# Kernel optimization log

Hardware: AMD Instinct MI355X
Metric: run time of the kernel (lower is better)

## Reference

```python
import jax, jax.numpy as jnp
import numpy as np

NUM_BLOCKS = 4
SPARSITY = 0.01
SCALE = 0.02


def _softshrink(x, lambd):
    return jnp.where(x > lambd, x - lambd, jnp.where(x < -lambd, x + lambd, 0.0))


def setup_inputs() -> dict:
    key = jax.random.key(0)
    k = jax.random.split(key, 5)
    B, N, C = 8, 4096, 768
    bs = C // NUM_BLOCKS
    return {
        "x": jax.random.normal(k[0], (B, N, C), dtype=jnp.float32),
        "complex_weight_1": jax.random.normal(k[1], (2, NUM_BLOCKS, bs, bs), dtype=jnp.float32) * SCALE,
        "complex_bias_1": jax.random.normal(k[2], (2, NUM_BLOCKS, bs), dtype=jnp.float32) * SCALE,
        "complex_weight_2": jax.random.normal(k[3], (2, NUM_BLOCKS, bs, bs), dtype=jnp.float32) * SCALE,
        "complex_bias_2": jax.random.normal(k[4], (2, NUM_BLOCKS, bs), dtype=jnp.float32) * SCALE,
    }


def reference(x, complex_weight_1, complex_bias_1, complex_weight_2, complex_bias_2):
    B, N, C = x.shape
    bs = C // NUM_BLOCKS
    xb = x.reshape(B, N, NUM_BLOCKS, bs)
    # FFT over (seq, block) axes, ortho norm -> complex64
    xf = jnp.fft.fft2(xb, axes=(1, 2), norm="ortho")

    mul = lambda t, w: jnp.einsum("snbd,bdk->snbk", t, w)

    w1, b1 = complex_weight_1, complex_bias_1
    w2, b2 = complex_weight_2, complex_bias_2

    xr, xi = xf.real, xf.imag
    r1 = jax.nn.relu(mul(xr, w1[0]) - mul(xi, w1[1]) + b1[0])
    i1 = jax.nn.relu(mul(xr, w1[1]) + mul(xi, w1[0]) + b1[1])
    r2 = mul(r1, w2[0]) - mul(i1, w2[1]) + b2[0]
    i2 = mul(r1, w2[1]) + mul(i1, w2[0]) + b2[1]

    r2 = _softshrink(r2, SPARSITY)
    i2 = _softshrink(i2, SPARSITY)

    z = jax.lax.complex(r2, i2)
    out = jnp.fft.ifft2(z, axes=(1, 2), norm="ortho").real.astype(jnp.float32)
    return out.reshape(B, N, C)
```

## Files before the change

kernel.cpp:

```cpp
#include <hip/hip_runtime.h>
#include <math.h>

#define N_SEQ   4096
#define C_TOT   768
#define NBLK    4
#define BS      192
#define B_BATCH 8
#define LAMBDA  0.01f
#define KTOT    384
#define APITCH  392
#define SW(x)   ((x) ^ (((x) >> 5) & 31))

typedef short    bf16x8  __attribute__((ext_vector_type(8)));
typedef short    short4v __attribute__((ext_vector_type(4)));
typedef float    f32x4   __attribute__((ext_vector_type(4)));
typedef unsigned short ushort_t;

__device__ __forceinline__ unsigned short f2bf(float f) {
  unsigned int u = __float_as_uint(f);
  u = (u + 0x7FFFu + ((u >> 16) & 1u)) >> 16;
  return (unsigned short)u;
}
__device__ __forceinline__ float b2f(unsigned short h) {
  return __uint_as_float(((unsigned int)h) << 16);
}

__device__ __forceinline__ void stockham_soa4(float* Ar, float* Ai,
                                              float* Br, float* Bi,
                                              int t, float sign) {
  float *sr = Ar, *si = Ai, *dr = Br, *di = Bi;
  float inv_p = 1.0f;
  int p = 1;
#pragma unroll
  for (int s = 0; s < 6; s++) {
#pragma unroll
    for (int m = 0; m < 2; m++) {
      int i = t + m * 512;
      int k = i & (p - 1);
      float a0r = sr[SW(i)],        a0i = si[SW(i)];
      float a1r = sr[SW(i + 1024)], a1i = si[SW(i + 1024)];
      float a2r = sr[SW(i + 2048)], a2i = si[SW(i + 2048)];
      float a3r = sr[SW(i + 3072)], a3i = si[SW(i + 3072)];
      float ang = sign * 1.5707963268f * inv_p * (float)k;
      float s1, c1;
      __sincosf(ang, &s1, &c1);
      float c2 = c1 * c1 - s1 * s1, s2 = 2.0f * c1 * s1;
      float c3 = c1 * c2 - s1 * s2, s3 = c1 * s2 + s1 * c2;
      float b1r = c1 * a1r - s1 * a1i, b1i = c1 * a1i + s1 * a1r;
      float b2r = c2 * a2r - s2 * a2i, b2i = c2 * a2i + s2 * a2r;
      float b3r = c3 * a3r - s3 * a3i, b3i = c3 * a3i + s3 * a3r;
      float t0r = a0r + b2r, t0i = a0i + b2i;
      float t1r = a0r - b2r, t1i = a0i - b2i;
      float t2r = b1r + b3r, t2i = b1i + b3i;
      float t3r = b1r - b3r, t3i = b1i - b3i;
      int j = ((i - k) << 2) + k;
      dr[SW(j)]         = t0r + t2r;        di[SW(j)]         = t0i + t2i;
      dr[SW(j + p)]     = t1r - sign * t3i; di[SW(j + p)]     = t1i + sign * t3r;
      dr[SW(j + 2 * p)] = t0r - t2r;        di[SW(j + 2 * p)] = t0i - t2i;
      dr[SW(j + 3 * p)] = t1r + sign * t3i; di[SW(j + 3 * p)] = t1i - sign * t3r;
    }
    __syncthreads();
    float* tp;
    tp = sr; sr = dr; dr = tp;
    tp = si; si = di; di = tp;
    p <<= 2;
    inv_p *= 0.25f;
  }
}

__global__ __launch_bounds__(256) void transpose_kernel(
    const float* __restrict__ src, float* __restrict__ dst, int R, int C) {
  __shared__ float tile[64][65];
  const int c0 = blockIdx.x * 64, r0 = blockIdx.y * 64, b = blockIdx.z;
  const int tid = threadIdx.x;
#pragma unroll
  for (int it = 0; it < 4; it++) {
    int g = it * 256 + tid;
    int r = g >> 4, q = g & 15;
    float4 v = *(const float4*)(src + ((size_t)b * R + r0 + r) * C + c0 + q * 4);
    tile[q * 4 + 0][r] = v.x;
    tile[q * 4 + 1][r] = v.y;
    tile[q * 4 + 2][r] = v.z;
    tile[q * 4 + 3][r] = v.w;
  }
  __syncthreads();
#pragma unroll
  for (int it = 0; it < 4; it++) {
    int g = it * 256 + tid;
    int c = g >> 4, w = g & 15;
    float4 v = make_float4(tile[c][w * 4 + 0], tile[c][w * 4 + 1],
                           tile[c][w * 4 + 2], tile[c][w * 4 + 3]);
    *(float4*)(dst + ((size_t)b * C + c0 + c) * R + r0 + w * 4) = v;
  }
}

__global__ __launch_bounds__(256) void prep_kernel(
    const float* __restrict__ w1, const float* __restrict__ w2,
    ushort_t* __restrict__ Bc) {
  int idx = blockIdx.x * 256 + threadIdx.x;
  int layer = idx / 589824; int r = idx - layer * 589824;
  int kb = r / 147456;      int r2 = r - kb * 147456;
  int jc = r2 / 6144;       int r3 = r2 - jc * 6144;
  int kc = r3 / 512;        int r4 = r3 - kc * 512;
  int lane = r4 >> 3;       int e = r4 & 7;
  int j = jc * 16 + (lane & 15);
  int k = kc * 32 + (lane >> 4) * 8 + e;
  const float* w = layer ? w2 : w1;
  float v;
  if (k < 192) {
    v = (j < 192) ? w[(kb * 192 + k) * 192 + j]
                  : w[((4 + kb) * 192 + k) * 192 + (j - 192)];
  } else {
    int k2 = k - 192;
    v = (j < 192) ? -w[((4 + kb) * 192 + k2) * 192 + j]
                  :  w[(kb * 192 + k2) * 192 + (j - 192)];
  }
  Bc[idx] = f2bf(v);
}

__global__ __launch_bounds__(512) void fft_fwd_kernel(
    const float* __restrict__ xT, ushort_t* __restrict__ Fr,
    ushort_t* __restrict__ Fi) {
  __shared__ float Ar[N_SEQ], Ai[N_SEQ], Br[N_SEQ], Bi[N_SEQ];
  const int q = blockIdx.x, b = blockIdx.y;
  const int c1 = 2 * q;
  const int t = threadIdx.x;
  const float* p1 = xT + ((size_t)b * C_TOT + c1) * N_SEQ;
  const float* p2 = p1 + N_SEQ;
#pragma unroll
  for (int m = 0; m < 8; m++) {
    int i = t + m * 512;
    Ar[SW(i)] = p1[i];
    Ai[SW(i)] = p2[i];
  }
  __syncthreads();
  stockham_soa4(Ar, Ai, Br, Bi, t, -1.0f);
  ushort_t* fr1 = Fr + ((size_t)b * C_TOT + c1) * N_SEQ;
  ushort_t* fi1 = Fi + ((size_t)b * C_TOT + c1) * N_SEQ;
#pragma unroll
  for (int m = 0; m < 8; m++) {
    int k = t + m * 512;
    int km = (N_SEQ - k) & (N_SEQ - 1);
    float a = Ar[SW(k)], bb = Ai[SW(k)], c = Ar[SW(km)], d = Ai[SW(km)];
    fr1[k]         = f2bf(0.5f * (a + c));
    fi1[k]         = f2bf(0.5f * (bb - d));
    fr1[N_SEQ + k] = f2bf(0.5f * (bb + d));
    fi1[N_SEQ + k] = f2bf(0.5f * (c - a));
  }
}

__global__ __launch_bounds__(256, 3) void mlp_kernel(
    const ushort_t* __restrict__ Fr, const ushort_t* __restrict__ Fi,
    const ushort_t* __restrict__ Bc,
    const float* __restrict__ b1g, const float* __restrict__ b2g,
    ushort_t* __restrict__ Or, ushort_t* __restrict__ Oi) {
  __shared__ ushort_t Abuf[64 * APITCH];
  const int nt = blockIdx.x, kb = blockIdx.y, b = blockIdx.z;
  const int n0 = nt * 64;
  const int tid = threadIdx.x;
  const int lane = tid & 63, wave = tid >> 6;
  const int fr = lane & 15, fg = lane >> 4;
  const int col0 = wave * 96;

  {
    const size_t S = (size_t)BS * N_SEQ;
    const float s = 0.0078125f;
#pragma unroll
    for (int it = 0; it < 6; it++) {
      int g = it * 256 + tid;
      int d = g >> 3, n8 = g & 7;
      size_t bse = ((size_t)(b * C_TOT + d)) * N_SEQ + n0 + n8 * 8;
      bf16x8 y0r = *(const bf16x8*)(Fr + bse);
      bf16x8 y0i = *(const bf16x8*)(Fi + bse);
      bf16x8 y1r = *(const bf16x8*)(Fr + bse + S);
      bf16x8 y1i = *(const bf16x8*)(Fi + bse + S);
      bf16x8 y2r = *(const bf16x8*)(Fr + bse + 2 * S);
      bf16x8 y2i = *(const bf16x8*)(Fi + bse + 2 * S);
      bf16x8 y3r = *(const bf16x8*)(Fr + bse + 3 * S);
      bf16x8 y3i = *(const bf16x8*)(Fi + bse + 3 * S);
#pragma unroll
      for (int e = 0; e < 8; e++) {
        float a0r = b2f((unsigned short)y0r[e]), a0i = b2f((unsigned short)y0i[e]);
        float a1r = b2f((unsigned short)y1r[e]), a1i = b2f((unsigned short)y1i[e]);
        float a2r = b2f((unsigned short)y2r[e]), a2i = b2f((unsigned short)y2i[e]);
        float a3r = b2f((unsigned short)y3r[e]), a3i = b2f((unsigned short)y3i[e]);
        float zr, zi;
        if (kb == 0)      { zr = a0r + a1r + a2r + a3r; zi = a0i + a1i + a2i + a3i; }
        else if (kb == 1) { zr = a0r + a1i - a2r - a3i; zi = a0i - a1r - a2i + a3r; }
        else if (kb == 2) { zr = a0r - a1r + a2r - a3r; zi = a0i - a1i + a2i - a3i; }
        else              { zr = a0r - a1i - a2r + a3i; zi = a0i + a1r - a2i - a3r; }
        int n = n8 * 8 + e;
        Abuf[n * APITCH + d]       = f2bf(zr * s);
        Abuf[n * APITCH + 192 + d] = f2bf(zi * s);
      }
    }
  }
  __syncthreads();

  const ushort_t* B1 = Bc + (size_t)kb * 147456 + (size_t)wave * 36864 +
                       (size_t)lane * 8;
  const ushort_t* B2 = B1 + 589824;

  f32x4 acc[4][6];
  bf16x8 bf0[6], bf1[6], afr[4];

  auto loadB = [&](const ushort_t* Bb, int kc, bf16x8* dst) {
#pragma unroll
    for (int ct = 0; ct < 6; ct++)
      dst[ct] = *(const bf16x8*)(Bb + (size_t)kc * 512 + ct * 6144);
  };
  auto doK = [&](int kc, bf16x8* bw) {
#pragma unroll
    for (int rt = 0; rt < 4; rt++)
      afr[rt] = *(const bf16x8*)(&Abuf[(rt * 16 + fr) * APITCH + kc * 32 + fg * 8]);
#pragma unroll
    for (int rt = 0; rt < 4; rt++)
#pragma unroll
      for (int ct = 0; ct < 6; ct++)
        acc[rt][ct] = __builtin_amdgcn_mfma_f32_16x16x32_bf16(
            afr[rt], bw[ct], acc[rt][ct], 0, 0, 0);
  };

#pragma unroll
  for (int rt = 0; rt < 4; rt++)
#pragma unroll
    for (int ct = 0; ct < 6; ct++) acc[rt][ct] = 0.0f;
  loadB(B1, 0, bf0);
#pragma unroll
  for (int kc2 = 0; kc2 < 6; kc2++) {
    loadB(B1, 2 * kc2 + 1, bf1);
    doK(2 * kc2, bf0);
    if (kc2 < 5) loadB(B1, 2 * kc2 + 2, bf0);
    doK(2 * kc2 + 1, bf1);
  }

  __syncthreads();
#pragma unroll
  for (int ct = 0; ct < 6; ct++) {
    int j = col0 + ct * 16 + fr;
    float bias = (j < 192) ? b1g[kb * 192 + j] : b1g[768 + kb * 192 + (j - 192)];
#pragma unroll
    for (int rt = 0; rt < 4; rt++)
#pragma unroll
      for (int reg = 0; reg < 4; reg++) {
        float v = acc[rt][ct][reg] + bias;
        v = fmaxf(v, 0.0f);
        Abuf[(rt * 16 + fg * 4 + reg) * APITCH + j] = f2bf(v);
      }
  }
  __syncthreads();

#pragma unroll
  for (int rt = 0; rt < 4; rt++)
#pragma unroll
    for (int ct = 0; ct < 6; ct++) acc[rt][ct] = 0.0f;
  loadB(B2, 0, bf0);
#pragma unroll
  for (int kc2 = 0; kc2 < 6; kc2++) {
    loadB(B2, 2 * kc2 + 1, bf1);
    doK(2 * kc2, bf0);
    if (kc2 < 5) loadB(B2, 2 * kc2 + 2, bf0);
    doK(2 * kc2 + 1, bf1);
  }

#pragma unroll
  for (int ct = 0; ct < 6; ct++) {
    int j = col0 + ct * 16 + fr;
    float bias;
    ushort_t* plane;
    if (j < 192) {
      bias = b2g[kb * 192 + j];
      plane = Or + ((size_t)(b * C_TOT + kb * 192 + j)) * N_SEQ;
    } else {
      bias = b2g[768 + kb * 192 + (j - 192)];
      plane = Oi + ((size_t)(b * C_TOT + kb * 192 + (j - 192))) * N_SEQ;
    }
#pragma unroll
    for (int rt = 0; rt < 4; rt++) {
      short4v pk;
#pragma unroll
      for (int reg = 0; reg < 4; reg++) {
        float v = acc[rt][ct][reg] + bias;
        v = (v > LAMBDA) ? (v - LAMBDA) : ((v < -LAMBDA) ? (v + LAMBDA) : 0.0f);
        pk[reg] = (short)f2bf(v);
      }
      *(short4v*)(plane + n0 + rt * 16 + fg * 4) = pk;
    }
  }
}

__global__ __launch_bounds__(512) void fft_inv_kernel(
    const ushort_t* __restrict__ Or, const ushort_t* __restrict__ Oi,
    float* __restrict__ yT) {
  __shared__ float Ar[N_SEQ], Ai[N_SEQ], Br[N_SEQ], Bi[N_SEQ];
  const int q = blockIdx.x, b = blockIdx.y;
  const int c1 = 2 * q;
  const int jb = c1 / 192;
  const int d  = c1 - jb * 192;
  const int t = threadIdx.x;
  const size_t S = (size_t)BS * N_SEQ;
  const float s = 1.0f / 128.0f;
  const size_t base0 = ((size_t)b * C_TOT + d) * N_SEQ;
#pragma unroll
  for (int m = 0; m < 2; m++) {
    int i0 = m * 2048 + t * 4;
#pragma unroll
    for (int col = 0; col < 2; col++) {
      size_t bse = base0 + (size_t)col * N_SEQ + i0;
      short4v z0r = *(const short4v*)(Or + bse);
      short4v z0i = *(const short4v*)(Oi + bse);
      short4v z1r = *(const short4v*)(Or + bse + S);
      short4v z1i = *(const short4v*)(Oi + bse + S);
      short4v z2r = *(const short4v*)(Or + bse + 2 * S);
      short4v z2i = *(const short4v*)(Oi + bse + 2 * S);
      short4v z3r = *(const short4v*)(Or + bse + 3 * S);
      short4v z3i = *(const short4v*)(Oi + bse + 3 * S);
      float* Dr = col ? Br : Ar;
      float* Di = col ? Bi : Ai;
#pragma unroll
      for (int e = 0; e < 4; e++) {
        float a0r = b2f((unsigned short)z0r[e]), a0i = b2f((unsigned short)z0i[e]);
        float a1r = b2f((unsigned short)z1r[e]), a1i = b2f((unsigned short)z1i[e]);
        float a2r = b2f((unsigned short)z2r[e]), a2i = b2f((unsigned short)z2i[e]);
        float a3r = b2f((unsigned short)z3r[e]), a3i = b2f((unsigned short)z3i[e]);
        float orr, oii;
        if (jb == 0)      { orr = a0r + a1r + a2r + a3r; oii = a0i + a1i + a2i + a3i; }
        else if (jb == 1) { orr = a0r - a1i - a2r + a3i; oii = a0i + a1r - a2i - a3r; }
        else if (jb == 2) { orr = a0r - a1r + a2r - a3r; oii = a0i - a1i + a2i - a3i; }
        else              { orr = a0r + a1i - a2r - a3i; oii = a0i - a1r - a2i + a3r; }
        int i = i0 + e;
        Dr[SW(i)] = orr * s;
        Di[SW(i)] = oii * s;
      }
    }
  }
  __syncthreads();
  float wr[8], wi[8];
#pragma unroll
  for (int m = 0; m < 8; m++) {
    int k = t + m * 512;
    int km = (N_SEQ - k) & (N_SEQ - 1);
    float zh1r = 0.5f * (Ar[SW(k)] + Ar[SW(km)]);
    float zh1i = 0.5f * (Ai[SW(k)] - Ai[SW(km)]);
    float zh2r = 0.5f * (Br[SW(k)] + Br[SW(km)]);
    float zh2i = 0.5f * (Bi[SW(k)] - Bi[SW(km)]);
    wr[m] = zh1r - zh2i;
    wi[m] = zh1i + zh2r;
  }
  __syncthreads();
#pragma unroll
  for (int m = 0; m < 8; m++) {
    int k = t + m * 512;
    Ar[SW(k)] = wr[m];
    Ai[SW(k)] = wi[m];
  }
  __syncthreads();
  stockham_soa4(Ar, Ai, Br, Bi, t, +1.0f);
  float* y1 = yT + ((size_t)b * C_TOT + c1) * N_SEQ;
#pragma unroll
  for (int m = 0; m < 8; m++) {
    int i = t + m * 512;
    y1[i]         = Ar[SW(i)];
    y1[N_SEQ + i] = Ai[SW(i)];
  }
}

extern "C" void kernel_launch(void* const* d_in, const int* in_sizes, int n_in,
                              void* d_out, int out_size, void* d_ws, size_t ws_size,
                              hipStream_t stream) {
  const float* x  = (const float*)d_in[0];
  const float* w1 = (const float*)d_in[1];
  const float* b1 = (const float*)d_in[2];
  const float* w2 = (const float*)d_in[3];
  const float* b2 = (const float*)d_in[4];
  float* out = (float*)d_out;

  const size_t P = (size_t)B_BATCH * C_TOT * N_SEQ;
  const size_t need = 8 * P + 2 * 589824 * sizeof(ushort_t);
  if (ws_size < need) return;
  char* base = (char*)d_ws;
  ushort_t* Fr = (ushort_t*)base;
  ushort_t* Fi = (ushort_t*)(base + 2 * P);
  float*    xT = (float*)(base + 4 * P);
  ushort_t* Or = (ushort_t*)(base + 4 * P);
  ushort_t* Oi = (ushort_t*)(base + 6 * P);
  float*    yT = (float*)base;
  ushort_t* Bc = (ushort_t*)(base + 8 * P);

  hipLaunchKernelGGL(prep_kernel, dim3(4608), dim3(256), 0, stream, w1, w2, Bc);
  hipLaunchKernelGGL(transpose_kernel, dim3(C_TOT / 64, N_SEQ / 64, B_BATCH),
                     dim3(256), 0, stream, x, xT, N_SEQ, C_TOT);
  hipLaunchKernelGGL(fft_fwd_kernel, dim3(C_TOT / 2, B_BATCH), dim3(512), 0,
                     stream, xT, Fr, Fi);
  hipLaunchKernelGGL(mlp_kernel, dim3(N_SEQ / 64, NBLK, B_BATCH), dim3(256),
                     0, stream, Fr, Fi, Bc, b1, b2, Or, Oi);
  hipLaunchKernelGGL(fft_inv_kernel, dim3(C_TOT / 2, B_BATCH), dim3(512), 0,
                     stream, Or, Oi, yT);
  hipLaunchKernelGGL(transpose_kernel, dim3(N_SEQ / 64, C_TOT / 64, B_BATCH),
                     dim3(256), 0, stream, yT, out, C_TOT, N_SEQ);
}
```

Before: 428.6 us.

## Switch FFT to radix-8 Stockham, swizzle MLP LDS tile, raise FFT occupancy

Replaces the radix-4 Stockham FFT (6 stages, 2 butterflies per thread) with a radix-8 version (4 stages, 1 butterfly per thread). This cuts the number of LDS round trips and barriers in the forward and inverse FFT kernels. It also XOR-swizzles the MLP kernel's activation tile columns by row to reduce LDS bank conflicts on MFMA fragment loads. It adds a min-blocks hint to the FFT kernels, which may cost register pressure because the radix-8 butterfly keeps many values live.

```diff
diff --git a/kernel.cpp b/kernel.cpp
--- a/kernel.cpp
+++ b/kernel.cpp
@@ -10,6 +10,7 @@
 #define KTOT    384
 #define APITCH  392
 #define SW(x)   ((x) ^ (((x) >> 5) & 31))
+#define ASWZ(row, col) ((col) ^ ((row) & 56))
 
 typedef short    bf16x8  __attribute__((ext_vector_type(8)));
 typedef short    short4v __attribute__((ext_vector_type(4)));
@@ -25,46 +26,74 @@
   return __uint_as_float(((unsigned int)h) << 16);
 }
 
-__device__ __forceinline__ void stockham_soa4(float* Ar, float* Ai,
+__device__ __forceinline__ void stockham_soa8(float* Ar, float* Ai,
                                               float* Br, float* Bi,
                                               int t, float sign) {
   float *sr = Ar, *si = Ai, *dr = Br, *di = Bi;
   float inv_p = 1.0f;
   int p = 1;
-#pragma unroll
-  for (int s = 0; s < 6; s++) {
-#pragma unroll
-    for (int m = 0; m < 2; m++) {
-      int i = t + m * 512;
-      int k = i & (p - 1);
-      float a0r = sr[SW(i)],        a0i = si[SW(i)];
-      float a1r = sr[SW(i + 1024)], a1i = si[SW(i + 1024)];
-      float a2r = sr[SW(i + 2048)], a2i = si[SW(i + 2048)];
-      float a3r = sr[SW(i + 3072)], a3i = si[SW(i + 3072)];
-      float ang = sign * 1.5707963268f * inv_p * (float)k;
-      float s1, c1;
-      __sincosf(ang, &s1, &c1);
-      float c2 = c1 * c1 - s1 * s1, s2 = 2.0f * c1 * s1;
-      float c3 = c1 * c2 - s1 * s2, s3 = c1 * s2 + s1 * c2;
-      float b1r = c1 * a1r - s1 * a1i, b1i = c1 * a1i + s1 * a1r;
-      float b2r = c2 * a2r - s2 * a2i, b2i = c2 * a2i + s2 * a2r;
-      float b3r = c3 * a3r - s3 * a3i, b3i = c3 * a3i + s3 * a3r;
-      float t0r = a0r + b2r, t0i = a0i + b2i;
-      float t1r = a0r - b2r, t1i = a0i - b2i;
-      float t2r = b1r + b3r, t2i = b1i + b3i;
-      float t3r = b1r - b3r, t3i = b1i - b3i;
-      int j = ((i - k) << 2) + k;
-      dr[SW(j)]         = t0r + t2r;        di[SW(j)]         = t0i + t2i;
-      dr[SW(j + p)]     = t1r - sign * t3i; di[SW(j + p)]     = t1i + sign * t3r;
-      dr[SW(j + 2 * p)] = t0r - t2r;        di[SW(j + 2 * p)] = t0i - t2i;
-      dr[SW(j + 3 * p)] = t1r + sign * t3i; di[SW(j + 3 * p)] = t1i - sign * t3r;
-    }
+  const float C8 = 0.70710678118f;
+#pragma unroll
+  for (int s = 0; s < 4; s++) {
+    int k = t & (p - 1);
+    float x0r = sr[SW(t)],        x0i = si[SW(t)];
+    float x1r = sr[SW(t + 512)],  x1i = si[SW(t + 512)];
+    float x2r = sr[SW(t + 1024)], x2i = si[SW(t + 1024)];
+    float x3r = sr[SW(t + 1536)], x3i = si[SW(t + 1536)];
+    float x4r = sr[SW(t + 2048)], x4i = si[SW(t + 2048)];
+    float x5r = sr[SW(t + 2560)], x5i = si[SW(t + 2560)];
+    float x6r = sr[SW(t + 3072)], x6i = si[SW(t + 3072)];
+    float x7r = sr[SW(t + 3584)], x7i = si[SW(t + 3584)];
+    float ang = sign * 0.78539816340f * inv_p * (float)k;
+    float s1, c1;
+    __sincosf(ang, &s1, &c1);
+    float c2 = c1 * c1 - s1 * s1, s2 = 2.0f * c1 * s1;
+    float c3 = c1 * c2 - s1 * s2, s3 = c1 * s2 + s1 * c2;
+    float c4 = c2 * c2 - s2 * s2, s4 = 2.0f * c2 * s2;
+    float c5 = c2 * c3 - s2 * s3, s5 = c2 * s3 + s2 * c3;
+    float c6 = c3 * c3 - s3 * s3, s6 = 2.0f * c3 * s3;
+    float c7 = c3 * c4 - s3 * s4, s7 = c3 * s4 + s3 * c4;
+    float b1r = c1 * x1r - s1 * x1i, b1i = c1 * x1i + s1 * x1r;
+    float b2r = c2 * x2r - s2 * x2i, b2i = c2 * x2i + s2 * x2r;
+    float b3r = c3 * x3r - s3 * x3i, b3i = c3 * x3i + s3 * x3r;
+    float b4r = c4 * x4r - s4 * x4i, b4i = c4 * x4i + s4 * x4r;
+    float b5r = c5 * x5r - s5 * x5i, b5i = c5 * x5i + s5 * x5r;
+    float b6r = c6 * x6r - s6 * x6i, b6i = c6 * x6i + s6 * x6r;
+    float b7r = c7 * x7r - s7 * x7i, b7i = c7 * x7i + s7 * x7r;
+    float et0r = x0r + b4r, et0i = x0i + b4i;
+    float et1r = x0r - b4r, et1i = x0i - b4i;
+    float et2r = b2r + b6r, et2i = b2i + b6i;
+    float et3r = b2r - b6r, et3i = b2i - b6i;
+    float E0r = et0r + et2r,        E0i = et0i + et2i;
+    float E1r = et1r - sign * et3i, E1i = et1i + sign * et3r;
+    float E2r = et0r - et2r,        E2i = et0i - et2i;
+    float E3r = et1r + sign * et3i, E3i = et1i - sign * et3r;
+    float ot0r = b1r + b5r, ot0i = b1i + b5i;
+    float ot1r = b1r - b5r, ot1i = b1i - b5i;
+    float ot2r = b3r + b7r, ot2i = b3i + b7i;
+    float ot3r = b3r - b7r, ot3i = b3i - b7i;
+    float O0r = ot0r + ot2r,        O0i = ot0i + ot2i;
+    float O1r = ot1r - sign * ot3i, O1i = ot1i + sign * ot3r;
+    float O2r = ot0r - ot2r,        O2i = ot0i - ot2i;
+    float O3r = ot1r + sign * ot3i, O3i = ot1i - sign * ot3r;
+    float u1r = C8 * (O1r - sign * O1i), u1i = C8 * (O1i + sign * O1r);
+    float u2r = -sign * O2i,             u2i = sign * O2r;
+    float u3r = -C8 * (O3r + sign * O3i), u3i = C8 * (sign * O3r - O3i);
+    int j = ((t - k) << 3) + k;
+    dr[SW(j)]         = E0r + O0r;  di[SW(j)]         = E0i + O0i;
+    dr[SW(j + p)]     = E1r + u1r;  di[SW(j + p)]     = E1i + u1i;
+    dr[SW(j + 2 * p)] = E2r + u2r;  di[SW(j + 2 * p)] = E2i + u2i;
+    dr[SW(j + 3 * p)] = E3r + u3r;  di[SW(j + 3 * p)] = E3i + u3i;
+    dr[SW(j + 4 * p)] = E0r - O0r;  di[SW(j + 4 * p)] = E0i - O0i;
+    dr[SW(j + 5 * p)] = E1r - u1r;  di[SW(j + 5 * p)] = E1i - u1i;
+    dr[SW(j + 6 * p)] = E2r - u2r;  di[SW(j + 6 * p)] = E2i - u2i;
+    dr[SW(j + 7 * p)] = E3r - u3r;  di[SW(j + 7 * p)] = E3i - u3i;
     __syncthreads();
     float* tp;
     tp = sr; sr = dr; dr = tp;
     tp = si; si = di; di = tp;
-    p <<= 2;
-    inv_p *= 0.25f;
+    p <<= 3;
+    inv_p *= 0.125f;
   }
 }
 
@@ -118,7 +147,7 @@
   Bc[idx] = f2bf(v);
 }
 
-__global__ __launch_bounds__(512) void fft_fwd_kernel(
+__global__ __launch_bounds__(512, 4) void fft_fwd_kernel(
     const float* __restrict__ xT, ushort_t* __restrict__ Fr,
     ushort_t* __restrict__ Fi) {
   __shared__ float Ar[N_SEQ], Ai[N_SEQ], Br[N_SEQ], Bi[N_SEQ];
@@ -134,7 +163,7 @@
     Ai[SW(i)] = p2[i];
   }
   __syncthreads();
-  stockham_soa4(Ar, Ai, Br, Bi, t, -1.0f);
+  stockham_soa8(Ar, Ai, Br, Bi, t, -1.0f);
   ushort_t* fr1 = Fr + ((size_t)b * C_TOT + c1) * N_SEQ;
   ushort_t* fi1 = Fi + ((size_t)b * C_TOT + c1) * N_SEQ;
 #pragma unroll
@@ -190,8 +219,8 @@
         else if (kb == 2) { zr = a0r - a1r + a2r - a3r; zi = a0i - a1i + a2i - a3i; }
         else              { zr = a0r - a1i - a2r + a3i; zi = a0i + a1r - a2i - a3r; }
         int n = n8 * 8 + e;
-        Abuf[n * APITCH + d]       = f2bf(zr * s);
-        Abuf[n * APITCH + 192 + d] = f2bf(zi * s);
+        Abuf[n * APITCH + ASWZ(n, d)]       = f2bf(zr * s);
+        Abuf[n * APITCH + 192 + ASWZ(n, d)] = f2bf(zi * s);
       }
     }
   }
@@ -211,8 +240,11 @@
   };
   auto doK = [&](int kc, bf16x8* bw) {
 #pragma unroll
-    for (int rt = 0; rt < 4; rt++)
-      afr[rt] = *(const bf16x8*)(&Abuf[(rt * 16 + fr) * APITCH + kc * 32 + fg * 8]);
+    for (int rt = 0; rt < 4; rt++) {
+      int arow = rt * 16 + fr;
+      afr[rt] = *(const bf16x8*)(
+          &Abuf[arow * APITCH + ASWZ(arow, kc * 32 + fg * 8)]);
+    }
 #pragma unroll
     for (int rt = 0; rt < 4; rt++)
 #pragma unroll
@@ -245,7 +277,8 @@
       for (int reg = 0; reg < 4; reg++) {
         float v = acc[rt][ct][reg] + bias;
         v = fmaxf(v, 0.0f);
-        Abuf[(rt * 16 + fg * 4 + reg) * APITCH + j] = f2bf(v);
+        int hrow = rt * 16 + fg * 4 + reg;
+        Abuf[hrow * APITCH + ASWZ(hrow, j)] = f2bf(v);
       }
   }
   __syncthreads();
@@ -289,7 +322,7 @@
   }
 }
 
-__global__ __launch_bounds__(512) void fft_inv_kernel(
+__global__ __launch_bounds__(512, 4) void fft_inv_kernel(
     const ushort_t* __restrict__ Or, const ushort_t* __restrict__ Oi,
     float* __restrict__ yT) {
   __shared__ float Ar[N_SEQ], Ai[N_SEQ], Br[N_SEQ], Bi[N_SEQ];
@@ -355,7 +388,7 @@
     Ai[SW(k)] = wi[m];
   }
   __syncthreads();
-  stockham_soa4(Ar, Ai, Br, Bi, t, +1.0f);
+  stockham_soa8(Ar, Ai, Br, Bi, t, +1.0f);
   float* y1 = yT + ((size_t)b * C_TOT + c1) * N_SEQ;
 #pragma unroll
   for (int m = 0; m < 8; m++) {
```

Result: slower. 529.3 us (+23.5%).
